# Performance work log

Hardware: AMD Instinct MI355X
Metric: run time of the kernel (lower is better)

Reference implementation:

```python
import jax, jax.numpy as jnp
import numpy as np
from jax import lax

DIM, D_INNER, D_STATE, D_CONV, DT_RANK = 256, 512, 16, 4, 16
B_, H_, W_ = 4, 64, 64


def setup_inputs() -> dict:
    key = jax.random.key(0)
    ks = jax.random.split(key, 10)
    s = lambda k, shape, scale: (jax.random.normal(k, shape, dtype=jnp.float32) * scale)
    inp = {
        "x": s(ks[0], (B_, DIM, H_, W_), 1.0),
        "in_proj_w": s(ks[1], (2 * D_INNER, DIM), DIM ** -0.5),
        "conv_w": s(ks[2], (D_INNER, 1, D_CONV), D_CONV ** -0.5),
        "conv_b": s(ks[3], (D_INNER,), 0.02),
        "x_proj_w": s(ks[4], (DT_RANK + 2 * D_STATE, D_INNER), D_INNER ** -0.5),
        "dt_proj_w": s(ks[5], (D_INNER, DT_RANK), DT_RANK ** -0.5),
        "dt_proj_b": s(ks[6], (D_INNER,), 0.02),
        # A_log init: log(arange(1..d_state)) broadcast over channels (standard S4D-real init)
        "A_log": jnp.broadcast_to(jnp.log(jnp.arange(1, D_STATE + 1, dtype=jnp.float32)), (D_INNER, D_STATE)).copy(),
        "D": jnp.ones((D_INNER,), dtype=jnp.float32),
        "out_proj_w": s(ks[7], (DIM, D_INNER), D_INNER ** -0.5),
    }
    return inp


def _mamba_forward(x, in_proj_w, conv_w, conv_b, x_proj_w, dt_proj_w, dt_proj_b, A_log, D, out_proj_w):
    b, c, h, w = x.shape
    L = h * w
    xs = x.reshape(b, c, L).transpose(0, 2, 1)                      # [b, L, dim]

    xz = jnp.einsum('bld,ed->ble', xs, in_proj_w)                   # [b, L, 2*d_inner]
    u, res = jnp.split(xz, 2, axis=-1)                              # each [b, L, d_inner]

    # causal depthwise conv1d over sequence
    u_t = u.transpose(0, 2, 1)                                      # [b, d_inner, L]
    u_t = lax.conv_general_dilated(u_t, conv_w, window_strides=(1,),
                                   padding=[(D_CONV - 1, 0)],
                                   feature_group_count=D_INNER,
                                   dimension_numbers=('NCH', 'OIH', 'NCH'))
    u = jax.nn.silu(u_t.transpose(0, 2, 1) + conv_b)                # [b, L, d_inner]

    dbc = jnp.einsum('bld,ed->ble', u, x_proj_w)                    # [b, L, dt_rank+2n]
    dt, Bm, Cm = jnp.split(dbc, [DT_RANK, DT_RANK + D_STATE], axis=-1)
    delta = jax.nn.softplus(jnp.einsum('blr,dr->bld', dt, dt_proj_w) + dt_proj_b)  # [b,L,d_inner]

    A = -jnp.exp(A_log)                                             # [d_inner, n]
    deltaA = jnp.exp(jnp.einsum('bld,dn->bldn', delta, A))          # [b,L,d,n]
    deltaBu = jnp.einsum('bld,bln,bld->bldn', delta, Bm, u)         # [b,L,d,n]

    def step(state, inp):
        dA, dBu, c_t = inp                                          # [b,d,n],[b,d,n],[b,n]
        state = dA * state + dBu
        y = jnp.einsum('bdn,bn->bd', state, c_t)
        return state, y

    init = jnp.zeros((b, D_INNER, D_STATE), dtype=x.dtype)
    _, ys = lax.scan(step, init, (jnp.moveaxis(deltaA, 1, 0),
                                  jnp.moveaxis(deltaBu, 1, 0),
                                  jnp.moveaxis(Cm, 1, 0)))
    y = jnp.moveaxis(ys, 0, 1) + u * D                              # [b, L, d_inner]
    y = y * jax.nn.silu(res)
    out = jnp.einsum('ble,de->bld', y, out_proj_w)                  # [b, L, dim]
    return out.transpose(0, 2, 1).reshape(b, c, h, w)


def reference(x, in_proj_w, conv_w, conv_b, x_proj_w, dt_proj_w, dt_proj_b, A_log, D, out_proj_w):
    return _mamba_forward(x, in_proj_w, conv_w, conv_b, x_proj_w, dt_proj_w, dt_proj_b, A_log, D, out_proj_w)
```

## Files before the change

kernel.cpp:

```cpp
#include <hip/hip_runtime.h>
#include <math.h>


namespace {
constexpr int kB   = 4;
constexpr int kDim = 256;
constexpr int kL   = 4096;
constexpr int kDI  = 512;
constexpr int kN   = 16;
constexpr int kNC  = 128;
constexpr int kCS  = 32;
}

typedef __attribute__((ext_vector_type(8))) short bf16x8;
typedef __attribute__((ext_vector_type(4))) float f32x4;
typedef __attribute__((ext_vector_type(2))) float f32x2;

__device__ __forceinline__ float rcpf(float x) { return __builtin_amdgcn_rcpf(x); }
__device__ __forceinline__ float siluf(float x) { return x * rcpf(1.f + __expf(-x)); }
__device__ __forceinline__ float softplusf(float x) {
  return fmaxf(x, 0.f) + __logf(1.f + __expf(-fabsf(x)));
}

__device__ __forceinline__ unsigned short f2bf(float x) {
  union { float f; unsigned int u; } v; v.f = x;
  unsigned int u = v.u;
  u += 0x7fffu + ((u >> 16) & 1u);
  return (unsigned short)(u >> 16);
}
__device__ __forceinline__ float bf2f(unsigned short u) {
  union { unsigned int i; float f; } v; v.i = ((unsigned int)u) << 16; return v.f;
}

__device__ __forceinline__ void gload_lds16(const void* g, void* l) {
  __builtin_amdgcn_global_load_lds(
      (const __attribute__((address_space(1))) unsigned int*)g,
      (__attribute__((address_space(3))) unsigned int*)l, 16, 0, 0);
}

__global__ __launch_bounds__(256) void k_wcvt(const float* __restrict__ w_in,
                                              const float* __restrict__ w_out,
                                              const float* __restrict__ w_x,
                                              const float* __restrict__ w_dt,
                                              unsigned short* __restrict__ wib,
                                              unsigned short* __restrict__ wob,
                                              unsigned short* __restrict__ wxb,
                                              unsigned short* __restrict__ wdtb,
                                              unsigned int* __restrict__ flag) {
  int idx = blockIdx.x * 256 + threadIdx.x;
  if (idx == 0) *flag = 0xFFFFFFFFu;
  if (idx < 262144) wib[idx] = f2bf(w_in[idx]);
  else if (idx < 393216) wob[idx - 262144] = f2bf(w_out[idx - 262144]);
  else if (idx < 417792) wxb[idx - 393216] = f2bf(w_x[idx - 393216]);
  else if (idx < 450560) {
    int i = idx - 417792;
    int r = i & 31, d = i >> 5;
    wdtb[i] = (r < 16) ? f2bf(w_dt[d * 16 + r]) : (unsigned short)0;
  }
}

__global__ __launch_bounds__(256) void k_aprep(const float* __restrict__ A_log,
                                               float* __restrict__ Avz,
                                               unsigned int* __restrict__ flag) {
  int d = blockIdx.x * 256 + threadIdx.x;
  float a0 = -__expf(A_log[d * kN]);
  bool ok = true;
#pragma unroll
  for (int n = 1; n < kN; ++n) {
    float av = -__expf(A_log[d * kN + n]);
    ok = ok && (fabsf(av - (n + 1) * a0) <= 1e-5f * fabsf(av));
  }
  Avz[d] = a0;
  if (!ok) atomicAnd(flag, 0u);
}

__global__ __launch_bounds__(256) void k_xt(const float* __restrict__ x,
                                            unsigned short* __restrict__ xt) {
  __shared__ float Xs[64][65];
  const int b = blockIdx.z, d0 = blockIdx.y * 64, l0 = blockIdx.x * 64;
  const int t = threadIdx.x, l = t & 63;
#pragma unroll
  for (int rep = 0; rep < 16; ++rep) {
    int dd = rep * 4 + (t >> 6);
    Xs[dd][l] = x[((size_t)b * kDim + d0 + dd) * kL + l0 + l];
  }
  __syncthreads();
#pragma unroll
  for (int rep = 0; rep < 8; ++rep) {
    int lj = rep * 8 + (t >> 5);
    int di = (t & 31) * 2;
    ushort2 v;
    v.x = f2bf(Xs[di][lj]);
    v.y = f2bf(Xs[di + 1][lj]);
    *(ushort2*)(xt + ((size_t)b * kL + l0 + lj) * kDim + d0 + di) = v;
  }
}

__global__ __launch_bounds__(256) void gemm_in_lm(const unsigned short* __restrict__ xt,
                                                  const unsigned short* __restrict__ W,
                                                  unsigned short* __restrict__ ubf,
                                                  unsigned short* __restrict__ resb) {
  __shared__ __align__(16) unsigned short As[128 * 64];
  __shared__ __align__(16) unsigned short Bs[128 * 64];
  const int e0 = blockIdx.x * 128;
  const int l0 = blockIdx.y * 128;
  const int b  = blockIdx.z;
  const int t  = threadIdx.x;
  const int wave = t >> 6, lane = t & 63;
  const int wm = wave >> 1, wn = wave & 1;
  const unsigned short* Ab = xt + (size_t)b * kL * kDim;

  f32x4 acc[4][4];
#pragma unroll
  for (int i = 0; i < 4; ++i)
#pragma unroll
    for (int j = 0; j < 4; ++j) acc[i][j] = (f32x4)0.0f;

  const int srow = t >> 3, sch = t & 7;
  for (int kt = 0; kt < 4; ++kt) {
    const int k0 = kt * 64;
#pragma unroll
    for (int c = 0; c < 4; ++c) {
      int row = c * 32 + srow;
      int gch = sch ^ (row & 7);
      gload_lds16(Ab + (size_t)(l0 + row) * kDim + k0 + gch * 8,
                  (char*)As + c * 4096 + wave * 1024);
      gload_lds16(W  + (size_t)(e0 + row) * kDim + k0 + gch * 8,
                  (char*)Bs + c * 4096 + wave * 1024);
    }
    __syncthreads();
#pragma unroll
    for (int ks = 0; ks < 2; ++ks) {
      bf16x8 af[4], bfr[4];
#pragma unroll
      for (int f = 0; f < 4; ++f) {
        int ra = wm * 64 + f * 16 + (lane & 15);
        int ca = (ks * 4 + (lane >> 4)) ^ (ra & 7);
        af[f] = *(const bf16x8*)((const char*)As + ra * 128 + ca * 16);
        int rb = wn * 64 + f * 16 + (lane & 15);
        int cb = (ks * 4 + (lane >> 4)) ^ (rb & 7);
        bfr[f] = *(const bf16x8*)((const char*)Bs + rb * 128 + cb * 16);
      }
#pragma unroll
      for (int i = 0; i < 4; ++i)
#pragma unroll
        for (int j = 0; j < 4; ++j)
          acc[i][j] = __builtin_amdgcn_mfma_f32_16x16x32_bf16(af[i], bfr[j], acc[i][j], 0, 0, 0);
    }
    __syncthreads();
  }

  const bool is_u = (e0 < kDI);
  unsigned short* dst = is_u ? ubf : resb;
  const int ebase = is_u ? e0 : (e0 - kDI);
#pragma unroll
  for (int i = 0; i < 4; ++i)
#pragma unroll
    for (int j = 0; j < 4; ++j)
#pragma unroll
      for (int r = 0; r < 4; ++r) {
        int l = l0 + wm * 64 + i * 16 + (lane >> 4) * 4 + r;
        int e = ebase + wn * 64 + j * 16 + (lane & 15);
        dst[((size_t)b * kL + l) * kDI + e] = f2bf(acc[i][j][r]);
      }
}

__global__ __launch_bounds__(256) void k_conv(const unsigned short* __restrict__ ubf,
                                              const float* __restrict__ cw,
                                              const float* __restrict__ cb,
                                              unsigned short* __restrict__ ucb) {
  int idx = blockIdx.x * 256 + threadIdx.x;
  int d8 = idx & 63;
  int l  = (idx >> 6) & (kL - 1);
  int b  = idx >> 18;
  int d0 = d8 * 8;
  const unsigned short* row = ubf + ((size_t)b * kL + l) * kDI + d0;
  uint4 zero = make_uint4(0, 0, 0, 0);
  uint4 c0 = *(const uint4*)row;
  uint4 c1 = (l >= 1) ? *(const uint4*)(row - kDI)     : zero;
  uint4 c2 = (l >= 2) ? *(const uint4*)(row - 2 * kDI) : zero;
  uint4 c3 = (l >= 3) ? *(const uint4*)(row - 3 * kDI) : zero;
  const unsigned int* p0 = (const unsigned int*)&c0;
  const unsigned int* p1 = (const unsigned int*)&c1;
  const unsigned int* p2 = (const unsigned int*)&c2;
  const unsigned int* p3 = (const unsigned int*)&c3;
  unsigned short ov[8];
#pragma unroll
  for (int c = 0; c < 8; ++c) {
    int q = c >> 1, hi = c & 1;
    float u0 = bf2f((unsigned short)(hi ? (p0[q] >> 16) : (p0[q] & 0xffff)));
    float u1 = bf2f((unsigned short)(hi ? (p1[q] >> 16) : (p1[q] & 0xffff)));
    float u2 = bf2f((unsigned short)(hi ? (p2[q] >> 16) : (p2[q] & 0xffff)));
    float u3 = bf2f((unsigned short)(hi ? (p3[q] >> 16) : (p3[q] & 0xffff)));
    float4 w = *(const float4*)(cw + (d0 + c) * 4);
    float acc = cb[d0 + c] + w.x * u3 + w.y * u2 + w.z * u1 + w.w * u0;
    ov[c] = f2bf(siluf(acc));
  }
  *(uint4*)(ucb + ((size_t)b * kL + l) * kDI + d0) = *(const uint4*)ov;
}

__global__ __launch_bounds__(256) void k_xproj(const unsigned short* __restrict__ Wx,
                                               const unsigned short* __restrict__ ucb,
                                               float* __restrict__ dbcBC,
                                               unsigned short* __restrict__ dtT) {
  __shared__ __align__(16) unsigned short As[64 * 64];
  __shared__ __align__(16) unsigned short Bs[128 * 64];
  const int l0 = blockIdx.x * 128;
  const int b  = blockIdx.y;
  const int t  = threadIdx.x;
  const int wave = t >> 6, lane = t & 63;
  const unsigned short* Bb = ucb + (size_t)b * kL * kDI;

  f32x4 acc[3][2];
#pragma unroll
  for (int i = 0; i < 3; ++i)
#pragma unroll
    for (int j = 0; j < 2; ++j) acc[i][j] = (f32x4)0.0f;

  const int srow = t >> 3, sch = t & 7;
  for (int kt = 0; kt < 8; ++kt) {
    const int k0 = kt * 64;
#pragma unroll
    for (int c = 0; c < 2; ++c) {
      int row = c * 32 + srow;
      int grow = row < 48 ? row : 47;
      int gch = sch ^ (row & 7);
      gload_lds16(Wx + (size_t)grow * kDI + k0 + gch * 8,
                  (char*)As + c * 4096 + wave * 1024);
    }
#pragma unroll
    for (int c = 0; c < 4; ++c) {
      int row = c * 32 + srow;
      int gch = sch ^ (row & 7);
      gload_lds16(Bb + (size_t)(l0 + row) * kDI + k0 + gch * 8,
                  (char*)Bs + c * 4096 + wave * 1024);
    }
    __syncthreads();
#pragma unroll
    for (int ks = 0; ks < 2; ++ks) {
      bf16x8 af[3], bfr[2];
#pragma unroll
      for (int f = 0; f < 3; ++f) {
        int ra = f * 16 + (lane & 15);
        int ca = (ks * 4 + (lane >> 4)) ^ (ra & 7);
        af[f] = *(const bf16x8*)((const char*)As + ra * 128 + ca * 16);
      }
#pragma unroll
      for (int f = 0; f < 2; ++f) {
        int rb = wave * 32 + f * 16 + (lane & 15);
        int cb = (ks * 4 + (lane >> 4)) ^ (rb & 7);
        bfr[f] = *(const bf16x8*)((const char*)Bs + rb * 128 + cb * 16);
      }
#pragma unroll
      for (int i = 0; i < 3; ++i)
#pragma unroll
        for (int j = 0; j < 2; ++j)
          acc[i][j] = __builtin_amdgcn_mfma_f32_16x16x32_bf16(af[i], bfr[j], acc[i][j], 0, 0, 0);
    }
    __syncthreads();
  }
#pragma unroll
  for (int i = 0; i < 3; ++i)
#pragma unroll
    for (int j = 0; j < 2; ++j)
#pragma unroll
      for (int r = 0; r < 4; ++r) {
        int m = i * 16 + (lane >> 4) * 4 + r;
        int l = l0 + wave * 32 + j * 16 + (lane & 15);
        if (i == 0) {
          size_t base = ((size_t)b * kL + l) * 32;
          dtT[base + m] = f2bf(acc[i][j][r]);
          dtT[base + m + 16] = 0;
        } else {
          dbcBC[((size_t)b * 32 + (m - 16)) * kL + l] = acc[i][j][r];
        }
      }
}

__global__ __launch_bounds__(256) void gemm_dt(const unsigned short* __restrict__ dtT,
                                               const unsigned short* __restrict__ Wdtb,
                                               const float* __restrict__ bdt,
                                               const float* __restrict__ Avz,
                                               const unsigned int* __restrict__ flag,
                                               const unsigned short* __restrict__ ucb,
                                               float* __restrict__ Ebuf,
                                               unsigned short* __restrict__ dub) {
  __shared__ __align__(16) unsigned short As[128 * 32];
  __shared__ __align__(16) unsigned short Bs[128 * 32];
  const int n0 = blockIdx.x * 128;
  const int l0 = blockIdx.y * 128;
  const int b  = blockIdx.z;
  const int t  = threadIdx.x;
  const int wave = t >> 6, lane = t & 63;
  const int wm = wave >> 1, wn = wave & 1;
  const unsigned short* Ab = dtT + (size_t)b * kL * 32;

  const int srow = t >> 2, sch = t & 3;
#pragma unroll
  for (int c = 0; c < 2; ++c) {
    int row = c * 64 + srow;
    int gch = sch ^ (row & 3);
    gload_lds16(Ab + (size_t)(l0 + row) * 32 + gch * 8,
                (char*)As + c * 4096 + t * 16);
    gload_lds16(Wdtb + (size_t)(n0 + row) * 32 + gch * 8,
                (char*)Bs + c * 4096 + t * 16);
  }
  __syncthreads();

  f32x4 acc[4][4];
#pragma unroll
  for (int i = 0; i < 4; ++i)
#pragma unroll
    for (int j = 0; j < 4; ++j) acc[i][j] = (f32x4)0.0f;

  bf16x8 af[4], bfr[4];
#pragma unroll
  for (int f = 0; f < 4; ++f) {
    int ra = wm * 64 + f * 16 + (lane & 15);
    int ca = (lane >> 4) ^ (ra & 3);
    af[f] = *(const bf16x8*)((const char*)As + ra * 64 + ca * 16);
    int rb = wn * 64 + f * 16 + (lane & 15);
    int cb = (lane >> 4) ^ (rb & 3);
    bfr[f] = *(const bf16x8*)((const char*)Bs + rb * 64 + cb * 16);
  }
#pragma unroll
  for (int i = 0; i < 4; ++i)
#pragma unroll
    for (int j = 0; j < 4; ++j)
      acc[i][j] = __builtin_amdgcn_mfma_f32_16x16x32_bf16(af[i], bfr[j], acc[i][j], 0, 0, 0);

  const bool fast = (*flag != 0u);
#pragma unroll
  for (int j = 0; j < 4; ++j) {
    int d = n0 + wn * 64 + j * 16 + (lane & 15);
    float bd = bdt[d];
    float av = Avz[d];
#pragma unroll
    for (int i = 0; i < 4; ++i)
#pragma unroll
      for (int r = 0; r < 4; ++r) {
        int l = l0 + wm * 64 + i * 16 + (lane >> 4) * 4 + r;
        size_t off = ((size_t)b * kL + l) * kDI + d;
        float delta = softplusf(acc[i][j][r] + bd);
        Ebuf[off] = fast ? __expf(delta * av) : delta;
        dub[off] = f2bf(delta * bf2f(ucb[off]));
      }
  }
}

__global__ __launch_bounds__(256) void k_scanA(const float* __restrict__ Ebuf,
                                               const unsigned short* __restrict__ dub,
                                               const unsigned short* __restrict__ ucb,
                                               const float* __restrict__ dbcBC,
                                               const float* __restrict__ A_log,
                                               const unsigned int* __restrict__ flag,
                                               float* __restrict__ P,
                                               float* __restrict__ S) {
  __shared__ __align__(16) float Bsh[16][kCS];
  const int b = blockIdx.z, ch = blockIdx.y;
  const int t = threadIdx.x;
  const int d = blockIdx.x * 256 + t;
  const int l0 = ch * kCS;
  {
    int row = t >> 4, li = (t & 15) * 2;
    *(float2*)&Bsh[row][li] =
        *(const float2*)&dbcBC[((size_t)b * 32 + row) * kL + l0 + li];
  }
  __syncthreads();
  const bool fast = (*flag != 0u);
  const float* pE = Ebuf + ((size_t)b * kL + l0) * kDI + d;
  const unsigned short* pDu = dub + ((size_t)b * kL + l0) * kDI + d;
  size_t obase = (size_t)(b * kNC + ch) * (kN * kDI) + d;

  if (fast) {
    f32x2 Sv2[8];
#pragma unroll
    for (int m = 0; m < 8; ++m) Sv2[m] = (f32x2){0.f, 0.f};
    float Pprod = 1.f;
    for (int i = 0; i < kCS; i += 4) {
      float E[4];
      f32x2 a2[4], e2[4], du2[4];
#pragma unroll
      for (int jj = 0; jj < 4; ++jj) {
        E[jj] = pE[(size_t)(i + jj) * kDI];
        float duv = bf2f(pDu[(size_t)(i + jj) * kDI]);
        du2[jj] = (f32x2){duv, duv};
        float Esq = E[jj] * E[jj];
        a2[jj] = (f32x2){E[jj], Esq};
        e2[jj] = (f32x2){Esq, Esq};
      }
      Pprod *= E[0] * E[1];
      Pprod *= E[2] * E[3];
#pragma unroll
      for (int m = 0; m < 8; ++m) {
        float4 Ba = *(const float4*)&Bsh[2 * m][i];
        float4 Bb = *(const float4*)&Bsh[2 * m + 1][i];
        Sv2[m] = Sv2[m] * a2[0] + du2[0] * (f32x2){Ba.x, Bb.x};
        Sv2[m] = Sv2[m] * a2[1] + du2[1] * (f32x2){Ba.y, Bb.y};
        Sv2[m] = Sv2[m] * a2[2] + du2[2] * (f32x2){Ba.z, Bb.z};
        Sv2[m] = Sv2[m] * a2[3] + du2[3] * (f32x2){Ba.w, Bb.w};
        if (m < 7) {
          a2[0] *= e2[0]; a2[1] *= e2[1]; a2[2] *= e2[2]; a2[3] *= e2[3];
        }
      }
    }
    float pw = Pprod;
#pragma unroll
    for (int n = 0; n < kN; ++n) {
      P[obase + (size_t)n * kDI] = pw;
      S[obase + (size_t)n * kDI] = (n & 1) ? Sv2[n >> 1].y : Sv2[n >> 1].x;
      pw *= Pprod;
    }
  } else {
    const unsigned short* pU = ucb + ((size_t)b * kL + l0) * kDI + d;
    float Av[16];
#pragma unroll
    for (int n = 0; n < kN; ++n) Av[n] = -__expf(A_log[d * kN + n]);
    float Pv[16], Sv[16];
#pragma unroll
    for (int n = 0; n < kN; ++n) { Pv[n] = 1.f; Sv[n] = 0.f; }
    for (int i = 0; i < kCS; i += 4) {
      float del[4], du[4];
#pragma unroll
      for (int jj = 0; jj < 4; ++jj) {
        del[jj] = pE[(size_t)(i + jj) * kDI];
        du[jj] = del[jj] * bf2f(pU[(size_t)(i + jj) * kDI]);
      }
#pragma unroll
      for (int n = 0; n < kN; ++n) {
        float4 B4 = *(const float4*)&Bsh[n][i];
        float a;
        a = __expf(del[0] * Av[n]); Pv[n] *= a; Sv[n] = Sv[n] * a + du[0] * B4.x;
        a = __expf(del[1] * Av[n]); Pv[n] *= a; Sv[n] = Sv[n] * a + du[1] * B4.y;
        a = __expf(del[2] * Av[n]); Pv[n] *= a; Sv[n] = Sv[n] * a + du[2] * B4.z;
        a = __expf(del[3] * Av[n]); Pv[n] *= a; Sv[n] = Sv[n] * a + du[3] * B4.w;
      }
    }
#pragma unroll
    for (int n = 0; n < kN; ++n) {
      P[obase + (size_t)n * kDI] = Pv[n];
      S[obase + (size_t)n * kDI] = Sv[n];
    }
  }
}

__global__ __launch_bounds__(256) void k_scanB(const float* __restrict__ P,
                                               const float* __restrict__ S,
                                               float* __restrict__ init) {
  int idx = blockIdx.x * 256 + threadIdx.x;
  int b = idx >> 13, nd = idx & 8191;
  size_t base = (size_t)b * kNC * 8192 + nd;
  float carry = 0.f;
  for (int c0 = 0; c0 < kNC; c0 += 8) {
    float p[8], s[8];
#pragma unroll
    for (int j = 0; j < 8; ++j) {
      size_t o = base + (size_t)(c0 + j) * 8192;
      p[j] = P[o]; s[j] = S[o];
    }
#pragma unroll
    for (int j = 0; j < 8; ++j) {
      init[base + (size_t)(c0 + j) * 8192] = carry;
      carry = p[j] * carry + s[j];
    }
  }
}

__global__ __launch_bounds__(256) void k_scanC(const float* __restrict__ Ebuf,
                                               const unsigned short* __restrict__ dub,
                                               const unsigned short* __restrict__ ucb,
                                               const float* __restrict__ dbcBC,
                                               const float* __restrict__ A_log,
                                               const unsigned int* __restrict__ flag,
                                               const float* __restrict__ init,
                                               const unsigned short* __restrict__ resb,
                                               const float* __restrict__ Dp,
                                               unsigned short* __restrict__ yt) {
  __shared__ __align__(16) float BCsh[32][kCS];
  const int b = blockIdx.z, ch = blockIdx.y;
  const int t = threadIdx.x;
  const int d = blockIdx.x * 256 + t;
  const int l0 = ch * kCS;
  {
    int row = t >> 3, li = (t & 7) * 4;
    *(float4*)&BCsh[row][li] =
        *(const float4*)&dbcBC[((size_t)b * 32 + row) * kL + l0 + li];
  }
  __syncthreads();
  const bool fast = (*flag != 0u);
  const float Dv = Dp[d];
  const float* pE = Ebuf + ((size_t)b * kL + l0) * kDI + d;
  const unsigned short* pDu = dub + ((size_t)b * kL + l0) * kDI + d;
  const unsigned short* pU = ucb + ((size_t)b * kL + l0) * kDI + d;
  const unsigned short* pR = resb + ((size_t)b * kL + l0) * kDI + d;
  unsigned short* pY = yt + ((size_t)b * kL + l0) * kDI + d;
  size_t ibase = (size_t)(b * kNC + ch) * (kN * kDI) + d;

  if (fast) {
    f32x2 s2[8];
#pragma unroll
    for (int m = 0; m < 8; ++m)
      s2[m] = (f32x2){init[ibase + (size_t)(2 * m) * kDI],
                      init[ibase + (size_t)(2 * m + 1) * kDI]};
    for (int i = 0; i < kCS; i += 4) {
      float uv[4];
      f32x2 a2[4], e2[4], du2[4], yacc2[4];
#pragma unroll
      for (int jj = 0; jj < 4; ++jj) {
        float E = pE[(size_t)(i + jj) * kDI];
        float duv = bf2f(pDu[(size_t)(i + jj) * kDI]);
        uv[jj] = bf2f(pU[(size_t)(i + jj) * kDI]);
        du2[jj] = (f32x2){duv, duv};
        float Esq = E * E;
        a2[jj] = (f32x2){E, Esq};
        e2[jj] = (f32x2){Esq, Esq};
        yacc2[jj] = (f32x2){0.f, 0.f};
      }
#pragma unroll
      for (int m = 0; m < 8; ++m) {
        float4 Ba = *(const float4*)&BCsh[2 * m][i];
        float4 Bb = *(const float4*)&BCsh[2 * m + 1][i];
        float4 Ca = *(const float4*)&BCsh[16 + 2 * m][i];
        float4 Cb = *(const float4*)&BCsh[16 + 2 * m + 1][i];
        s2[m] = s2[m] * a2[0] + du2[0] * (f32x2){Ba.x, Bb.x};
        yacc2[0] = yacc2[0] + s2[m] * (f32x2){Ca.x, Cb.x};
        s2[m] = s2[m] * a2[1] + du2[1] * (f32x2){Ba.y, Bb.y};
        yacc2[1] = yacc2[1] + s2[m] * (f32x2){Ca.y, Cb.y};
        s2[m] = s2[m] * a2[2] + du2[2] * (f32x2){Ba.z, Bb.z};
        yacc2[2] = yacc2[2] + s2[m] * (f32x2){Ca.z, Cb.z};
        s2[m] = s2[m] * a2[3] + du2[3] * (f32x2){Ba.w, Bb.w};
        yacc2[3] = yacc2[3] + s2[m] * (f32x2){Ca.w, Cb.w};
        if (m < 7) {
          a2[0] *= e2[0]; a2[1] *= e2[1]; a2[2] *= e2[2]; a2[3] *= e2[3];
        }
      }
#pragma unroll
      for (int jj = 0; jj < 4; ++jj) {
        float yv = yacc2[jj].x + yacc2[jj].y;
        float r = bf2f(pR[(size_t)(i + jj) * kDI]);
        float gv = (yv + uv[jj] * Dv) * siluf(r);
        pY[(size_t)(i + jj) * kDI] = f2bf(gv);
      }
    }
  } else {
    float Av[16];
#pragma unroll
    for (int n = 0; n < kN; ++n) Av[n] = -__expf(A_log[d * kN + n]);
    float s[16];
#pragma unroll
    for (int n = 0; n < kN; ++n) s[n] = init[ibase + (size_t)n * kDI];
    for (int i = 0; i < kCS; i += 4) {
      float uv[4], du[4], del[4], yacc[4] = {0.f, 0.f, 0.f, 0.f};
#pragma unroll
      for (int jj = 0; jj < 4; ++jj) {
        del[jj] = pE[(size_t)(i + jj) * kDI];
        uv[jj] = bf2f(pU[(size_t)(i + jj) * kDI]);
        du[jj] = del[jj] * uv[jj];
      }
#pragma unroll
      for (int n = 0; n < kN; ++n) {
        float4 B4 = *(const float4*)&BCsh[n][i];
        float4 C4 = *(const float4*)&BCsh[16 + n][i];
        float a;
        a = __expf(del[0] * Av[n]); s[n] = s[n] * a + du[0] * B4.x; yacc[0] += s[n] * C4.x;
        a = __expf(del[1] * Av[n]); s[n] = s[n] * a + du[1] * B4.y; yacc[1] += s[n] * C4.y;
        a = __expf(del[2] * Av[n]); s[n] = s[n] * a + du[2] * B4.z; yacc[2] += s[n] * C4.z;
        a = __expf(del[3] * Av[n]); s[n] = s[n] * a + du[3] * B4.w; yacc[3] += s[n] * C4.w;
      }
#pragma unroll
      for (int jj = 0; jj < 4; ++jj) {
        float r = bf2f(pR[(size_t)(i + jj) * kDI]);
        float gv = (yacc[jj] + uv[jj] * Dv) * siluf(r);
        pY[(size_t)(i + jj) * kDI] = f2bf(gv);
      }
    }
  }
}

__global__ __launch_bounds__(256) void gemm_out(const unsigned short* __restrict__ A,
                                                const unsigned short* __restrict__ Bt,
                                                float* __restrict__ C0) {
  __shared__ __align__(16) unsigned short As[128 * 64];
  __shared__ __align__(16) unsigned short Bs[128 * 64];
  const int n0 = blockIdx.x * 128;
  const int m0 = blockIdx.y * 128;
  const int b  = blockIdx.z;
  const int t  = threadIdx.x;
  const int wave = t >> 6, lane = t & 63;
  const int wm = wave >> 1, wn = wave & 1;
  const unsigned short* Bb = Bt + (size_t)b * kL * kDI;

  f32x4 acc[4][4];
#pragma unroll
  for (int i = 0; i < 4; ++i)
#pragma unroll
    for (int j = 0; j < 4; ++j) acc[i][j] = (f32x4)0.0f;

  const int srow = t >> 3, sch = t & 7;
  for (int kt = 0; kt < 8; ++kt) {
    const int k0 = kt * 64;
#pragma unroll
    for (int c = 0; c < 4; ++c) {
      int row = c * 32 + srow;
      int gch = sch ^ (row & 7);
      gload_lds16(A  + (size_t)(m0 + row) * kDI + k0 + gch * 8,
                  (char*)As + c * 4096 + wave * 1024);
      gload_lds16(Bb + (size_t)(n0 + row) * kDI + k0 + gch * 8,
                  (char*)Bs + c * 4096 + wave * 1024);
    }
    __syncthreads();
#pragma unroll
    for (int ks = 0; ks < 2; ++ks) {
      bf16x8 af[4], bfr[4];
#pragma unroll
      for (int f = 0; f < 4; ++f) {
        int ra = wm * 64 + f * 16 + (lane & 15);
        int ca = (ks * 4 + (lane >> 4)) ^ (ra & 7);
        af[f] = *(const bf16x8*)((const char*)As + ra * 128 + ca * 16);
        int rb = wn * 64 + f * 16 + (lane & 15);
        int cb = (ks * 4 + (lane >> 4)) ^ (rb & 7);
        bfr[f] = *(const bf16x8*)((const char*)Bs + rb * 128 + cb * 16);
      }
#pragma unroll
      for (int i = 0; i < 4; ++i)
#pragma unroll
        for (int j = 0; j < 4; ++j)
          acc[i][j] = __builtin_amdgcn_mfma_f32_16x16x32_bf16(af[i], bfr[j], acc[i][j], 0, 0, 0);
    }
    __syncthreads();
  }
#pragma unroll
  for (int i = 0; i < 4; ++i)
#pragma unroll
    for (int j = 0; j < 4; ++j)
#pragma unroll
      for (int r = 0; r < 4; ++r) {
        int m = m0 + wm * 64 + i * 16 + (lane >> 4) * 4 + r;
        int n = n0 + wn * 64 + j * 16 + (lane & 15);
        C0[((size_t)b * kDim + m) * kL + n] = acc[i][j][r];
      }
}

extern "C" void kernel_launch(void* const* d_in, const int* in_sizes, int n_in,
                              void* d_out, int out_size, void* d_ws, size_t ws_size,
                              hipStream_t stream) {
  const float* x       = (const float*)d_in[0];
  const float* in_w    = (const float*)d_in[1];
  const float* conv_w  = (const float*)d_in[2];
  const float* conv_b  = (const float*)d_in[3];
  const float* xproj_w = (const float*)d_in[4];
  const float* dt_w    = (const float*)d_in[5];
  const float* dt_b    = (const float*)d_in[6];
  const float* A_log   = (const float*)d_in[7];
  const float* Dp      = (const float*)d_in[8];
  const float* out_w   = (const float*)d_in[9];
  float* out = (float*)d_out;

  float* ws = (float*)d_ws;
  const size_t nBLD  = (size_t)kB * kL * kDI;
  const size_t nPS   = (size_t)kB * kNC * kN * kDI;
  float* dbcBC = ws;
  float* Pb    = dbcBC + 524288;
  float* Sb    = Pb + nPS;
  float* initb = Sb + nPS;
  float* Ebuf  = initb + nPS;
  unsigned short* ubf  = (unsigned short*)Ebuf;
  unsigned short* ucb  = (unsigned short*)(Ebuf + nBLD);
  unsigned short* resb = ucb + nBLD;
  unsigned short* dub  = resb + nBLD;
  unsigned short* xt   = dub;
  unsigned short* dtT  = dub + nBLD;
  unsigned short* wib  = dtT + 524288;
  unsigned short* wob  = wib + 262144;
  unsigned short* wxb  = wob + 131072;
  unsigned short* wdtb = wxb + 24576;
  float* Avz           = (float*)(wdtb + 32768);
  unsigned int* flag   = (unsigned int*)(Avz + 512);
  unsigned short* yt   = (unsigned short*)Pb;

  k_wcvt<<<dim3(1760), 256, 0, stream>>>(in_w, out_w, xproj_w, dt_w, wib, wob, wxb, wdtb, flag);
  k_aprep<<<dim3(2), 256, 0, stream>>>(A_log, Avz, flag);
  k_xt<<<dim3(kL / 64, kDim / 64, kB), 256, 0, stream>>>(x, xt);
  gemm_in_lm<<<dim3(8, kL / 128, kB), 256, 0, stream>>>(xt, wib, ubf, resb);
  k_conv<<<dim3((unsigned)(kB * kL * 64 / 256)), 256, 0, stream>>>(ubf, conv_w, conv_b, ucb);
  k_xproj<<<dim3(kL / 128, kB), 256, 0, stream>>>(wxb, ucb, dbcBC, dtT);
  gemm_dt<<<dim3(kDI / 128, kL / 128, kB), 256, 0, stream>>>(dtT, wdtb, dt_b, Avz, flag, ucb, Ebuf, dub);
  k_scanA<<<dim3(2, kNC, kB), 256, 0, stream>>>(Ebuf, dub, ucb, dbcBC, A_log, flag, Pb, Sb);
  k_scanB<<<dim3(kB * kDI * kN / 256), 256, 0, stream>>>(Pb, Sb, initb);
  k_scanC<<<dim3(2, kNC, kB), 256, 0, stream>>>(Ebuf, dub, ucb, dbcBC, A_log, flag, initb, resb, Dp, yt);
  gemm_out<<<dim3(kL / 128, kDim / 128, kB), 256, 0, stream>>>(wob, yt, out);
}
```

Before: 162.6 us.

## Fuse prep kernels and dt projection into x_proj; store bf16 delta instead of exp

Merges the weight conversion, A preparation and x transpose into a single prep launch, using per-block ballot flags instead of an atomic. Fuses the dt_proj GEMM and softplus into the x_proj kernel through shared memory, which removes the dtT round trip and one launch. It stores delta as bf16 rather than an fp32 exp(delta*A) buffer plus a separate delta*u buffer. The scan kernels then recompute the exp and delta*u, cutting global memory traffic at the cost of extra exp work and a serial dt GEMM loop inside fewer x_proj blocks.

After: 155.0 us. -4.7%, faster.

```diff
diff --git a/kernel.cpp b/kernel.cpp
--- a/kernel.cpp
+++ b/kernel.cpp
@@ -38,61 +38,71 @@
       (__attribute__((address_space(3))) unsigned int*)l, 16, 0, 0);
 }
 
-__global__ __launch_bounds__(256) void k_wcvt(const float* __restrict__ w_in,
+__global__ __launch_bounds__(256) void k_prep(const float* __restrict__ w_in,
                                               const float* __restrict__ w_out,
                                               const float* __restrict__ w_x,
                                               const float* __restrict__ w_dt,
+                                              const float* __restrict__ A_log,
+                                              const float* __restrict__ x,
                                               unsigned short* __restrict__ wib,
                                               unsigned short* __restrict__ wob,
                                               unsigned short* __restrict__ wxb,
                                               unsigned short* __restrict__ wdtb,
-                                              unsigned int* __restrict__ flag) {
-  int idx = blockIdx.x * 256 + threadIdx.x;
-  if (idx == 0) *flag = 0xFFFFFFFFu;
-  if (idx < 262144) wib[idx] = f2bf(w_in[idx]);
-  else if (idx < 393216) wob[idx - 262144] = f2bf(w_out[idx - 262144]);
-  else if (idx < 417792) wxb[idx - 393216] = f2bf(w_x[idx - 393216]);
-  else if (idx < 450560) {
-    int i = idx - 417792;
-    int r = i & 31, d = i >> 5;
-    wdtb[i] = (r < 16) ? f2bf(w_dt[d * 16 + r]) : (unsigned short)0;
-  }
-}
-
-__global__ __launch_bounds__(256) void k_aprep(const float* __restrict__ A_log,
-                                               float* __restrict__ Avz,
-                                               unsigned int* __restrict__ flag) {
-  int d = blockIdx.x * 256 + threadIdx.x;
-  float a0 = -__expf(A_log[d * kN]);
-  bool ok = true;
-#pragma unroll
-  for (int n = 1; n < kN; ++n) {
-    float av = -__expf(A_log[d * kN + n]);
-    ok = ok && (fabsf(av - (n + 1) * a0) <= 1e-5f * fabsf(av));
-  }
-  Avz[d] = a0;
-  if (!ok) atomicAnd(flag, 0u);
-}
-
-__global__ __launch_bounds__(256) void k_xt(const float* __restrict__ x,
-                                            unsigned short* __restrict__ xt) {
+                                              float* __restrict__ Avz,
+                                              unsigned int* __restrict__ flagA,
+                                              unsigned short* __restrict__ xt) {
   __shared__ float Xs[64][65];
-  const int b = blockIdx.z, d0 = blockIdx.y * 64, l0 = blockIdx.x * 64;
-  const int t = threadIdx.x, l = t & 63;
-#pragma unroll
-  for (int rep = 0; rep < 16; ++rep) {
-    int dd = rep * 4 + (t >> 6);
-    Xs[dd][l] = x[((size_t)b * kDim + d0 + dd) * kL + l0 + l];
-  }
-  __syncthreads();
-#pragma unroll
-  for (int rep = 0; rep < 8; ++rep) {
-    int lj = rep * 8 + (t >> 5);
-    int di = (t & 31) * 2;
-    ushort2 v;
-    v.x = f2bf(Xs[di][lj]);
-    v.y = f2bf(Xs[di + 1][lj]);
-    *(ushort2*)(xt + ((size_t)b * kL + l0 + lj) * kDim + d0 + di) = v;
+  const int blk = blockIdx.x;
+  const int t = threadIdx.x;
+  if (blk < 1760) {
+    int idx = blk * 256 + t;
+    if (idx < 262144) wib[idx] = f2bf(w_in[idx]);
+    else if (idx < 393216) wob[idx - 262144] = f2bf(w_out[idx - 262144]);
+    else if (idx < 417792) wxb[idx - 393216] = f2bf(w_x[idx - 393216]);
+    else {
+      int i = idx - 417792;
+      int r = i & 31, d = i >> 5;
+      wdtb[i] = (r < 16) ? f2bf(w_dt[d * 16 + r]) : (unsigned short)0;
+    }
+  } else if (blk < 1762) {
+    int d = (blk - 1760) * 256 + t;
+    float a0 = -__expf(A_log[d * kN]);
+    bool ok = true;
+#pragma unroll
+    for (int n = 1; n < kN; ++n) {
+      float av = -__expf(A_log[d * kN + n]);
+      ok = ok && (fabsf(av - (n + 1) * a0) <= 1e-5f * fabsf(av));
+    }
+    Avz[d] = a0;
+    unsigned long long bal = __ballot(ok);
+    int wv = t >> 6;
+    if ((t & 63) == 0) ((unsigned long long*)Xs)[wv] = bal;
+    __syncthreads();
+    if (t == 0) {
+      unsigned long long all = ~0ull;
+#pragma unroll
+      for (int w = 0; w < 4; ++w) all &= ((unsigned long long*)Xs)[w];
+      flagA[blk - 1760] = (all == ~0ull) ? 1u : 0u;
+    }
+  } else {
+    int id = blk - 1762;
+    int lb = id & 63, db = (id >> 6) & 3, b = id >> 8;
+    const int d0 = db * 64, l0 = lb * 64, l = t & 63;
+#pragma unroll
+    for (int rep = 0; rep < 16; ++rep) {
+      int dd = rep * 4 + (t >> 6);
+      Xs[dd][l] = x[((size_t)b * kDim + d0 + dd) * kL + l0 + l];
+    }
+    __syncthreads();
+#pragma unroll
+    for (int rep = 0; rep < 8; ++rep) {
+      int lj = rep * 8 + (t >> 5);
+      int di = (t & 31) * 2;
+      ushort2 v;
+      v.x = f2bf(Xs[di][lj]);
+      v.y = f2bf(Xs[di + 1][lj]);
+      *(ushort2*)(xt + ((size_t)b * kL + l0 + lj) * kDim + d0 + di) = v;
+    }
   }
 }
 
@@ -199,12 +209,16 @@
   *(uint4*)(ucb + ((size_t)b * kL + l) * kDI + d0) = *(const uint4*)ov;
 }
 
-__global__ __launch_bounds__(256) void k_xproj(const unsigned short* __restrict__ Wx,
-                                               const unsigned short* __restrict__ ucb,
-                                               float* __restrict__ dbcBC,
-                                               unsigned short* __restrict__ dtT) {
+__global__ __launch_bounds__(256) void k_xproj_dt(const unsigned short* __restrict__ Wx,
+                                                  const unsigned short* __restrict__ Wdtb,
+                                                  const float* __restrict__ bdt,
+                                                  float* __restrict__ dbcBC,
+                                                  const unsigned short* __restrict__ ucb,
+                                                  unsigned short* __restrict__ delb) {
   __shared__ __align__(16) unsigned short As[64 * 64];
   __shared__ __align__(16) unsigned short Bs[128 * 64];
+  __shared__ __align__(16) unsigned short dtTl[128 * 32];
+  __shared__ __align__(16) unsigned short Wl[128 * 32];
   const int l0 = blockIdx.x * 128;
   const int b  = blockIdx.y;
   const int t  = threadIdx.x;
@@ -259,101 +273,85 @@
     }
     __syncthreads();
   }
-#pragma unroll
-  for (int i = 0; i < 3; ++i)
+
+#pragma unroll
+  for (int i = 1; i < 3; ++i)
 #pragma unroll
     for (int j = 0; j < 2; ++j)
 #pragma unroll
       for (int r = 0; r < 4; ++r) {
         int m = i * 16 + (lane >> 4) * 4 + r;
         int l = l0 + wave * 32 + j * 16 + (lane & 15);
-        if (i == 0) {
-          size_t base = ((size_t)b * kL + l) * 32;
-          dtT[base + m] = f2bf(acc[i][j][r]);
-          dtT[base + m + 16] = 0;
-        } else {
-          dbcBC[((size_t)b * 32 + (m - 16)) * kL + l] = acc[i][j][r];
+        dbcBC[((size_t)b * 32 + (m - 16)) * kL + l] = acc[i][j][r];
+      }
+#pragma unroll
+  for (int j = 0; j < 2; ++j) {
+    int l = wave * 32 + j * 16 + (lane & 15);
+    int m0 = (lane >> 4) * 4;
+    ushort4 v;
+    v.x = f2bf(acc[0][j][0]); v.y = f2bf(acc[0][j][1]);
+    v.z = f2bf(acc[0][j][2]); v.w = f2bf(acc[0][j][3]);
+    int byte = l * 64 + (((m0 >> 3) ^ (l & 3)) << 4) + ((m0 & 7) << 1);
+    *(ushort4*)((char*)dtTl + byte) = v;
+  }
+  {
+    int lz = t >> 1, zc = 2 + (t & 1);
+    *(uint4*)((char*)dtTl + lz * 64 + ((zc ^ (lz & 3)) << 4)) = make_uint4(0, 0, 0, 0);
+  }
+  __syncthreads();
+
+  const int wl = wave >> 1, wd = wave & 1;
+  for (int dt4 = 0; dt4 < 4; ++dt4) {
+#pragma unroll
+    for (int c2 = 0; c2 < 2; ++c2) {
+      int unit = c2 * 256 + t;
+      int row = unit >> 2, sc = unit & 3;
+      int gch = sc ^ (row & 3);
+      gload_lds16(Wdtb + (size_t)(dt4 * 128 + row) * 32 + gch * 8,
+                  (char*)Wl + c2 * 4096 + t * 16);
+    }
+    __syncthreads();
+    f32x4 acc2[4][4];
+#pragma unroll
+    for (int i = 0; i < 4; ++i)
+#pragma unroll
+      for (int j = 0; j < 4; ++j) acc2[i][j] = (f32x4)0.0f;
+    bf16x8 afr[4], bfr2[4];
+#pragma unroll
+    for (int f = 0; f < 4; ++f) {
+      int ra = wl * 64 + f * 16 + (lane & 15);
+      afr[f] = *(const bf16x8*)((const char*)dtTl + ra * 64 + (((lane >> 4) ^ (ra & 3)) << 4));
+      int rb = wd * 64 + f * 16 + (lane & 15);
+      bfr2[f] = *(const bf16x8*)((const char*)Wl + rb * 64 + (((lane >> 4) ^ (rb & 3)) << 4));
+    }
+#pragma unroll
+    for (int i = 0; i < 4; ++i)
+#pragma unroll
+      for (int j = 0; j < 4; ++j)
+        acc2[i][j] = __builtin_amdgcn_mfma_f32_16x16x32_bf16(afr[i], bfr2[j], acc2[i][j], 0, 0, 0);
+#pragma unroll
+    for (int j = 0; j < 4; ++j) {
+      int d = dt4 * 128 + wd * 64 + j * 16 + (lane & 15);
+      float bd = bdt[d];
+#pragma unroll
+      for (int i = 0; i < 4; ++i)
+#pragma unroll
+        for (int r = 0; r < 4; ++r) {
+          int l = l0 + wl * 64 + i * 16 + (lane >> 4) * 4 + r;
+          float delta = softplusf(acc2[i][j][r] + bd);
+          delb[((size_t)b * kL + l) * kDI + d] = f2bf(delta);
         }
-      }
-}
-
-__global__ __launch_bounds__(256) void gemm_dt(const unsigned short* __restrict__ dtT,
-                                               const unsigned short* __restrict__ Wdtb,
-                                               const float* __restrict__ bdt,
-                                               const float* __restrict__ Avz,
-                                               const unsigned int* __restrict__ flag,
-                                               const unsigned short* __restrict__ ucb,
-                                               float* __restrict__ Ebuf,
-                                               unsigned short* __restrict__ dub) {
-  __shared__ __align__(16) unsigned short As[128 * 32];
-  __shared__ __align__(16) unsigned short Bs[128 * 32];
-  const int n0 = blockIdx.x * 128;
-  const int l0 = blockIdx.y * 128;
-  const int b  = blockIdx.z;
-  const int t  = threadIdx.x;
-  const int wave = t >> 6, lane = t & 63;
-  const int wm = wave >> 1, wn = wave & 1;
-  const unsigned short* Ab = dtT + (size_t)b * kL * 32;
-
-  const int srow = t >> 2, sch = t & 3;
-#pragma unroll
-  for (int c = 0; c < 2; ++c) {
-    int row = c * 64 + srow;
-    int gch = sch ^ (row & 3);
-    gload_lds16(Ab + (size_t)(l0 + row) * 32 + gch * 8,
-                (char*)As + c * 4096 + t * 16);
-    gload_lds16(Wdtb + (size_t)(n0 + row) * 32 + gch * 8,
-                (char*)Bs + c * 4096 + t * 16);
-  }
-  __syncthreads();
-
-  f32x4 acc[4][4];
-#pragma unroll
-  for (int i = 0; i < 4; ++i)
-#pragma unroll
-    for (int j = 0; j < 4; ++j) acc[i][j] = (f32x4)0.0f;
-
-  bf16x8 af[4], bfr[4];
-#pragma unroll
-  for (int f = 0; f < 4; ++f) {
-    int ra = wm * 64 + f * 16 + (lane & 15);
-    int ca = (lane >> 4) ^ (ra & 3);
-    af[f] = *(const bf16x8*)((const char*)As + ra * 64 + ca * 16);
-    int rb = wn * 64 + f * 16 + (lane & 15);
-    int cb = (lane >> 4) ^ (rb & 3);
-    bfr[f] = *(const bf16x8*)((const char*)Bs + rb * 64 + cb * 16);
-  }
-#pragma unroll
-  for (int i = 0; i < 4; ++i)
-#pragma unroll
-    for (int j = 0; j < 4; ++j)
-      acc[i][j] = __builtin_amdgcn_mfma_f32_16x16x32_bf16(af[i], bfr[j], acc[i][j], 0, 0, 0);
-
-  const bool fast = (*flag != 0u);
-#pragma unroll
-  for (int j = 0; j < 4; ++j) {
-    int d = n0 + wn * 64 + j * 16 + (lane & 15);
-    float bd = bdt[d];
-    float av = Avz[d];
-#pragma unroll
-    for (int i = 0; i < 4; ++i)
-#pragma unroll
-      for (int r = 0; r < 4; ++r) {
-        int l = l0 + wm * 64 + i * 16 + (lane >> 4) * 4 + r;
-        size_t off = ((size_t)b * kL + l) * kDI + d;
-        float delta = softplusf(acc[i][j][r] + bd);
-        Ebuf[off] = fast ? __expf(delta * av) : delta;
-        dub[off] = f2bf(delta * bf2f(ucb[off]));
-      }
-  }
-}
-
-__global__ __launch_bounds__(256) void k_scanA(const float* __restrict__ Ebuf,
-                                               const unsigned short* __restrict__ dub,
+    }
+    __syncthreads();
+  }
+}
+
+__global__ __launch_bounds__(256) void k_scanA(const unsigned short* __restrict__ delb,
                                                const unsigned short* __restrict__ ucb,
                                                const float* __restrict__ dbcBC,
                                                const float* __restrict__ A_log,
-                                               const unsigned int* __restrict__ flag,
+                                               const float* __restrict__ Avz,
+                                               const unsigned int* __restrict__ flagA,
                                                float* __restrict__ P,
                                                float* __restrict__ S) {
   __shared__ __align__(16) float Bsh[16][kCS];
@@ -367,9 +365,10 @@
         *(const float2*)&dbcBC[((size_t)b * 32 + row) * kL + l0 + li];
   }
   __syncthreads();
-  const bool fast = (*flag != 0u);
-  const float* pE = Ebuf + ((size_t)b * kL + l0) * kDI + d;
-  const unsigned short* pDu = dub + ((size_t)b * kL + l0) * kDI + d;
+  const bool fast = (flagA[0] != 0u) && (flagA[1] != 0u);
+  const float Av0 = Avz[d];
+  const unsigned short* pDel = delb + ((size_t)b * kL + l0) * kDI + d;
+  const unsigned short* pU = ucb + ((size_t)b * kL + l0) * kDI + d;
   size_t obase = (size_t)(b * kNC + ch) * (kN * kDI) + d;
 
   if (fast) {
@@ -378,19 +377,19 @@
     for (int m = 0; m < 8; ++m) Sv2[m] = (f32x2){0.f, 0.f};
     float Pprod = 1.f;
     for (int i = 0; i < kCS; i += 4) {
-      float E[4];
       f32x2 a2[4], e2[4], du2[4];
 #pragma unroll
       for (int jj = 0; jj < 4; ++jj) {
-        E[jj] = pE[(size_t)(i + jj) * kDI];
-        float duv = bf2f(pDu[(size_t)(i + jj) * kDI]);
+        float dl = bf2f(pDel[(size_t)(i + jj) * kDI]);
+        float uu = bf2f(pU[(size_t)(i + jj) * kDI]);
+        float E = __expf(dl * Av0);
+        float duv = dl * uu;
         du2[jj] = (f32x2){duv, duv};
-        float Esq = E[jj] * E[jj];
-        a2[jj] = (f32x2){E[jj], Esq};
+        float Esq = E * E;
+        a2[jj] = (f32x2){E, Esq};
         e2[jj] = (f32x2){Esq, Esq};
-      }
-      Pprod *= E[0] * E[1];
-      Pprod *= E[2] * E[3];
+        Pprod *= E;
+      }
 #pragma unroll
       for (int m = 0; m < 8; ++m) {
         float4 Ba = *(const float4*)&Bsh[2 * m][i];
@@ -412,7 +411,6 @@
       pw *= Pprod;
     }
   } else {
-    const unsigned short* pU = ucb + ((size_t)b * kL + l0) * kDI + d;
     float Av[16];
 #pragma unroll
     for (int n = 0; n < kN; ++n) Av[n] = -__expf(A_log[d * kN + n]);
@@ -423,7 +421,7 @@
       float del[4], du[4];
 #pragma unroll
       for (int jj = 0; jj < 4; ++jj) {
-        del[jj] = pE[(size_t)(i + jj) * kDI];
+        del[jj] = bf2f(pDel[(size_t)(i + jj) * kDI]);
         du[jj] = del[jj] * bf2f(pU[(size_t)(i + jj) * kDI]);
       }
 #pragma unroll
@@ -466,12 +464,12 @@
   }
 }
 
-__global__ __launch_bounds__(256) void k_scanC(const float* __restrict__ Ebuf,
-                                               const unsigned short* __restrict__ dub,
+__global__ __launch_bounds__(256) void k_scanC(const unsigned short* __restrict__ delb,
                                                const unsigned short* __restrict__ ucb,
                                                const float* __restrict__ dbcBC,
                                                const float* __restrict__ A_log,
-                                               const unsigned int* __restrict__ flag,
+                                               const float* __restrict__ Avz,
+                                               const unsigned int* __restrict__ flagA,
                                                const float* __restrict__ init,
                                                const unsigned short* __restrict__ resb,
                                                const float* __restrict__ Dp,
@@ -487,10 +485,10 @@
         *(const float4*)&dbcBC[((size_t)b * 32 + row) * kL + l0 + li];
   }
   __syncthreads();
-  const bool fast = (*flag != 0u);
+  const bool fast = (flagA[0] != 0u) && (flagA[1] != 0u);
+  const float Av0 = Avz[d];
   const float Dv = Dp[d];
-  const float* pE = Ebuf + ((size_t)b * kL + l0) * kDI + d;
-  const unsigned short* pDu = dub + ((size_t)b * kL + l0) * kDI + d;
+  const unsigned short* pDel = delb + ((size_t)b * kL + l0) * kDI + d;
   const unsigned short* pU = ucb + ((size_t)b * kL + l0) * kDI + d;
   const unsigned short* pR = resb + ((size_t)b * kL + l0) * kDI + d;
   unsigned short* pY = yt + ((size_t)b * kL + l0) * kDI + d;
@@ -507,9 +505,10 @@
       f32x2 a2[4], e2[4], du2[4], yacc2[4];
 #pragma unroll
       for (int jj = 0; jj < 4; ++jj) {
-        float E = pE[(size_t)(i + jj) * kDI];
-        float duv = bf2f(pDu[(size_t)(i + jj) * kDI]);
+        float dl = bf2f(pDel[(size_t)(i + jj) * kDI]);
         uv[jj] = bf2f(pU[(size_t)(i + jj) * kDI]);
+        float E = __expf(dl * Av0);
+        float duv = dl * uv[jj];
         du2[jj] = (f32x2){duv, duv};
         float Esq = E * E;
         a2[jj] = (f32x2){E, Esq};
@@ -553,7 +552,7 @@
       float uv[4], du[4], del[4], yacc[4] = {0.f, 0.f, 0.f, 0.f};
 #pragma unroll
       for (int jj = 0; jj < 4; ++jj) {
-        del[jj] = pE[(size_t)(i + jj) * kDI];
+        del[jj] = bf2f(pDel[(size_t)(i + jj) * kDI]);
         uv[jj] = bf2f(pU[(size_t)(i + jj) * kDI]);
         du[jj] = del[jj] * uv[jj];
       }
@@ -663,30 +662,26 @@
   float* Pb    = dbcBC + 524288;
   float* Sb    = Pb + nPS;
   float* initb = Sb + nPS;
-  float* Ebuf  = initb + nPS;
-  unsigned short* ubf  = (unsigned short*)Ebuf;
-  unsigned short* ucb  = (unsigned short*)(Ebuf + nBLD);
+  unsigned short* ubf  = (unsigned short*)(initb + nPS);
+  unsigned short* ucb  = ubf + nBLD;
   unsigned short* resb = ucb + nBLD;
-  unsigned short* dub  = resb + nBLD;
-  unsigned short* xt   = dub;
-  unsigned short* dtT  = dub + nBLD;
-  unsigned short* wib  = dtT + 524288;
+  unsigned short* delb = resb + nBLD;
+  unsigned short* wib  = delb + nBLD;
   unsigned short* wob  = wib + 262144;
   unsigned short* wxb  = wob + 131072;
   unsigned short* wdtb = wxb + 24576;
   float* Avz           = (float*)(wdtb + 32768);
-  unsigned int* flag   = (unsigned int*)(Avz + 512);
+  unsigned int* flagA  = (unsigned int*)(Avz + 512);
+  unsigned short* xt   = delb;
   unsigned short* yt   = (unsigned short*)Pb;
 
-  k_wcvt<<<dim3(1760), 256, 0, stream>>>(in_w, out_w, xproj_w, dt_w, wib, wob, wxb, wdtb, flag);
-  k_aprep<<<dim3(2), 256, 0, stream>>>(A_log, Avz, flag);
-  k_xt<<<dim3(kL / 64, kDim / 64, kB), 256, 0, stream>>>(x, xt);
+  k_prep<<<dim3(2786), 256, 0, stream>>>(in_w, out_w, xproj_w, dt_w, A_log, x,
+                                         wib, wob, wxb, wdtb, Avz, flagA, xt);
   gemm_in_lm<<<dim3(8, kL / 128, kB), 256, 0, stream>>>(xt, wib, ubf, resb);
   k_conv<<<dim3((unsigned)(kB * kL * 64 / 256)), 256, 0, stream>>>(ubf, conv_w, conv_b, ucb);
-  k_xproj<<<dim3(kL / 128, kB), 256, 0, stream>>>(wxb, ucb, dbcBC, dtT);
-  gemm_dt<<<dim3(kDI / 128, kL / 128, kB), 256, 0, stream>>>(dtT, wdtb, dt_b, Avz, flag, ucb, Ebuf, dub);
-  k_scanA<<<dim3(2, kNC, kB), 256, 0, stream>>>(Ebuf, dub, ucb, dbcBC, A_log, flag, Pb, Sb);
+  k_xproj_dt<<<dim3(kL / 128, kB), 256, 0, stream>>>(wxb, wdtb, dt_b, dbcBC, ucb, delb);
+  k_scanA<<<dim3(2, kNC, kB), 256, 0, stream>>>(delb, ucb, dbcBC, A_log, Avz, flagA, Pb, Sb);
   k_scanB<<<dim3(kB * kDI * kN / 256), 256, 0, stream>>>(Pb, Sb, initb);
-  k_scanC<<<dim3(2, kNC, kB), 256, 0, stream>>>(Ebuf, dub, ucb, dbcBC, A_log, flag, initb, resb, Dp, yt);
+  k_scanC<<<dim3(2, kNC, kB), 256, 0, stream>>>(delb, ucb, dbcBC, A_log, Avz, flagA, initb, resb, Dp, yt);
   gemm_out<<<dim3(kL / 128, kDim / 128, kB), 256, 0, stream>>>(wob, yt, out);
 }
```
